# Performance work log

Measured on AMD Instinct MI355X. Metric: run time of the kernel, lower is better.

Reference implementation:

```python
import jax, jax.numpy as jnp
import numpy as np

N_NODES = 16384
N_EDGES = 65536
B = 256
L = 1000
BN_EPS = 1e-5


def _bn_last(h, g, b, m, v):
    # BatchNorm1d in eval mode over last (feature) axis
    return (h - m) / jnp.sqrt(v + BN_EPS) * g + b


def _bn_chan(h, g, b, m, v):
    # BatchNorm1d in eval mode over channel axis of [N, C, W]
    inv = g / jnp.sqrt(v + BN_EPS)
    return (h - m[None, :, None]) * inv[None, :, None] + b[None, :, None]


def _conv1d(x, W, b):
    # x: [N, C, W], W: [O, I, K], stride 1, VALID
    y = jax.lax.conv_general_dilated(x, W, (1,), 'VALID',
                                     dimension_numbers=('NCH', 'OIH', 'NCH'))
    return y + b[None, :, None]


def _forward(x, g1_W1, g1_b1, g1_W2, g1_b2, gW1, gb1, gW2, gb2,
             bn_gamma, bn_beta, bn_mean, bn_var, fcxd_W, fcxd_b, embed,
             c1_W, c1_b, c2_W, c2_b, c3_W, c3_b,
             cbn_gamma, cbn_beta, cbn_mean, cbn_var, fcxc_W, fcxc_b,
             bnfc_gamma, bnfc_beta, bnfc_mean, bnfc_var,
             fc1_W, fc1_b, fc2_W, fc2_b, out_W, out_b,
             edge_index, batch, target):
    src, dst = edge_index[0], edge_index[1]
    # GIN layer 1: out_i = MLP(x_i + sum_{j->i} x_j)  (eps = 0)
    agg = jax.ops.segment_sum(x[src], dst, num_segments=N_NODES)
    h = x + agg
    h = jnp.maximum(h @ g1_W1 + g1_b1, 0.0) @ g1_W2 + g1_b2
    h = _bn_last(jnp.maximum(h, 0.0), bn_gamma[0], bn_beta[0], bn_mean[0], bn_var[0])
    # GIN layers 2..5 (stacked params)
    for i in range(4):
        agg = jax.ops.segment_sum(h[src], dst, num_segments=N_NODES)
        t = h + agg
        t = jnp.maximum(t @ gW1[i] + gb1[i], 0.0) @ gW2[i] + gb2[i]
        h = _bn_last(jnp.maximum(t, 0.0), bn_gamma[i + 1], bn_beta[i + 1],
                     bn_mean[i + 1], bn_var[i + 1])
    # global_add_pool over graph ids
    pooled = jax.ops.segment_sum(h, batch, num_segments=B)          # [B, 32]
    xd = jnp.maximum(pooled @ fcxd_W + fcxd_b, 0.0)                 # [B, 128] (dropout: eval)
    # protein branch
    emb = embed[target]                                             # [B, L, 128]
    xd2 = jnp.broadcast_to(xd[:, None, :], (B, L, xd.shape[-1]))
    xc = jnp.concatenate([emb, xd2], axis=-1).transpose(0, 2, 1)    # [B, 256, L]
    conv_params = [(c1_W, c1_b), (c2_W, c2_b), (c3_W, c3_b)]
    for i in range(3):
        xc = _conv1d(xc, conv_params[i][0], conv_params[i][1])
        xc = jnp.maximum(_bn_chan(xc, cbn_gamma[i], cbn_beta[i],
                                  cbn_mean[i], cbn_var[i]), 0.0)
    xcm = jnp.max(xc, axis=-1)                                      # global max pool -> [B, 32]
    xcf = jnp.maximum(_bn_last(xcm @ fcxc_W + fcxc_b,
                               bnfc_gamma, bnfc_beta, bnfc_mean, bnfc_var), 0.0)
    z = jnp.concatenate([xd, xcf], axis=1)                          # [B, 256]
    z = jnp.maximum(z @ fc1_W + fc1_b, 0.0)
    z = jnp.maximum(z @ fc2_W + fc2_b, 0.0)
    return z @ out_W + out_b                                        # [B, 1]


def setup_inputs() -> dict:
    key = jax.random.key(0)
    ks = list(jax.random.split(key, 48))
    it = iter(range(48))
    f32 = jnp.float32

    def rn(sh, s=0.1):
        return jax.random.normal(ks[next(it)], sh, dtype=f32) * s

    def un(sh):
        return jax.random.uniform(ks[next(it)], sh, dtype=f32, minval=0.5, maxval=1.5)

    inp = {}
    inp['x'] = jax.random.normal(ks[next(it)], (N_NODES, 78), dtype=f32)
    inp['edge_index'] = jax.random.randint(ks[next(it)], (2, N_EDGES), 0, N_NODES, dtype=jnp.int32)
    inp['batch'] = jnp.sort(jax.random.randint(ks[next(it)], (N_NODES,), 0, B, dtype=jnp.int32))
    inp['target'] = jax.random.randint(ks[next(it)], (B, L), 0, 26, dtype=jnp.int32)
    inp['g1_W1'] = rn((78, 32)); inp['g1_b1'] = rn((32,))
    inp['g1_W2'] = rn((32, 32)); inp['g1_b2'] = rn((32,))
    inp['gW1'] = rn((4, 32, 32)); inp['gb1'] = rn((4, 32))
    inp['gW2'] = rn((4, 32, 32)); inp['gb2'] = rn((4, 32))
    inp['bn_gamma'] = un((5, 32)); inp['bn_beta'] = rn((5, 32))
    inp['bn_mean'] = rn((5, 32)); inp['bn_var'] = un((5, 32))
    inp['fcxd_W'] = rn((32, 128)); inp['fcxd_b'] = rn((128,))
    inp['embed'] = rn((26, 128), 1.0)
    inp['c1_W'] = rn((32, 256, 16)); inp['c1_b'] = rn((32,))
    inp['c2_W'] = rn((32, 32, 16)); inp['c2_b'] = rn((32,))
    inp['c3_W'] = rn((32, 32, 16)); inp['c3_b'] = rn((32,))
    inp['cbn_gamma'] = un((3, 32)); inp['cbn_beta'] = rn((3, 32))
    inp['cbn_mean'] = rn((3, 32)); inp['cbn_var'] = un((3, 32))
    inp['fcxc_W'] = rn((32, 128)); inp['fcxc_b'] = rn((128,))
    inp['bnfc_gamma'] = un((128,)); inp['bnfc_beta'] = rn((128,))
    inp['bnfc_mean'] = rn((128,)); inp['bnfc_var'] = un((128,))
    inp['fc1_W'] = rn((256, 1024)); inp['fc1_b'] = rn((1024,))
    inp['fc2_W'] = rn((1024, 256)); inp['fc2_b'] = rn((256,))
    inp['out_W'] = rn((256, 1)); inp['out_b'] = rn((1,))
    return inp


def reference(x, edge_index, batch, target, g1_W1, g1_b1, g1_W2, g1_b2,
              gW1, gb1, gW2, gb2, bn_gamma, bn_beta, bn_mean, bn_var,
              fcxd_W, fcxd_b, embed, c1_W, c1_b, c2_W, c2_b, c3_W, c3_b,
              cbn_gamma, cbn_beta, cbn_mean, cbn_var, fcxc_W, fcxc_b,
              bnfc_gamma, bnfc_beta, bnfc_mean, bnfc_var,
              fc1_W, fc1_b, fc2_W, fc2_b, out_W, out_b):
    return _forward(x, g1_W1, g1_b1, g1_W2, g1_b2, gW1, gb1, gW2, gb2,
                    bn_gamma, bn_beta, bn_mean, bn_var, fcxd_W, fcxd_b, embed,
                    c1_W, c1_b, c2_W, c2_b, c3_W, c3_b,
                    cbn_gamma, cbn_beta, cbn_mean, cbn_var, fcxc_W, fcxc_b,
                    bnfc_gamma, bnfc_beta, bnfc_mean, bnfc_var,
                    fc1_W, fc1_b, fc2_W, fc2_b, out_W, out_b,
                    edge_index, batch, target)
```

## Files before the change

kernel.cpp:

```cpp
#include <hip/hip_runtime.h>
#include <hip/hip_bf16.h>

typedef __hip_bfloat16 bf16;
__device__ __forceinline__ float b2f(bf16 v){ return __bfloat162float(v); }

typedef __attribute__((ext_vector_type(8))) short s8v;
typedef __attribute__((ext_vector_type(4))) float f4v;

#define N_NODES 16384
#define N_EDGES 65536
#define NB 256
#define LSEQ 1000
#define BN_EPS 1e-5f
#define W1O 985
#define W2O 970
#define W3O 955

__device__ int g_isf32;

__device__ __forceinline__ float LD(const void* p, int i, int f){
    return f ? ((const float*)p)[i] : b2f(((const bf16*)p)[i]);
}

__device__ __forceinline__ unsigned short f2b(float x){
    unsigned u = __float_as_uint(x);
    return (unsigned short)((u + 0x7FFFu + ((u >> 16) & 1u)) >> 16);
}
__device__ __forceinline__ float bb2f(unsigned short h){
    return __uint_as_float(((unsigned)h) << 16);
}

__global__ void k_dtype(const void* x){
    if (threadIdx.x != 0 || blockIdx.x != 0) return;
    const unsigned short* u = (const unsigned short*)x;
    int insane = 0;
    for (int i = 0; i < 512; i++){
        unsigned short h = u[i];
        int ex = (h >> 7) & 0xFF;
        if (!(h == 0 || (ex >= 96 && ex <= 142))) insane++;
    }
    g_isf32 = (insane > 50) ? 1 : 0;
}

__device__ float g_hA[N_NODES*32];
__device__ float g_hB[N_NODES*32];
__device__ float g_xd[NB*128];
__device__ float g_P[16*26*32];
__device__ float g_wsum[32*128];
__device__ float g_xdb[NB*32];
__device__ float g_xcm[NB*32];
__device__ __attribute__((aligned(16))) unsigned short g_wf[2][32768];
__device__ int g_deg[N_NODES];
__device__ int g_cur[N_NODES];
__device__ int g_rowptr[N_NODES + 1];
__device__ int g_csrc[N_EDGES];
__device__ int g_gstart[NB + 1];

__global__ void k_zero(){
    int i = blockIdx.x*256 + threadIdx.x;
    if (i < N_NODES) g_deg[i] = 0;
    else g_xcm[i - N_NODES] = 0.f;
}

__global__ void k_count(const int* __restrict__ ei){
    int e = blockIdx.x*256 + threadIdx.x;
    atomicAdd(&g_deg[ei[N_EDGES + e]], 1);
}
__global__ __launch_bounds__(1024) void k_scan(){
    __shared__ int part[1024];
    int t = threadIdx.x;
    int base = t*16;
    int s = 0;
    #pragma unroll
    for (int i = 0; i < 16; i++) s += g_deg[base + i];
    part[t] = s;
    __syncthreads();
    for (int off = 1; off < 1024; off <<= 1){
        int v = (t >= off) ? part[t - off] : 0;
        __syncthreads();
        part[t] += v;
        __syncthreads();
    }
    int run = (t == 0) ? 0 : part[t - 1];
    for (int i = 0; i < 16; i++){
        g_rowptr[base + i] = run;
        g_cur[base + i] = run;
        run += g_deg[base + i];
    }
    if (t == 1023) g_rowptr[N_NODES] = run;
}
__global__ void k_fill(const int* __restrict__ ei){
    int e = blockIdx.x*256 + threadIdx.x;
    int d = ei[N_EDGES + e];
    int slot = atomicAdd(&g_cur[d], 1);
    g_csrc[slot] = ei[e];
}
__global__ void k_ranges(const int* __restrict__ batch){
    int b = threadIdx.x;
    int lo = 0, hi = N_NODES;
    while (lo < hi){ int mid = (lo + hi) >> 1; if (batch[mid] < b) lo = mid + 1; else hi = mid; }
    g_gstart[b] = lo;
    if (b == 0) g_gstart[NB] = N_NODES;
}

__global__ void k_wpack(const void* w2, const void* w3){
    const int F = g_isf32;
    int idx = blockIdx.x*256 + threadIdx.x;
    int sel = idx >> 15;
    int r = idx & 32767;
    int j = r & 7;
    int lane = (r >> 3) & 63;
    int hl = (r >> 9) & 1;
    int ogrp = (r >> 10) & 1;
    int ktg = r >> 11;
    int c = (lane >> 4)*8 + j;
    int o = ogrp*16 + (lane & 15);
    const void* Wt = sel ? w3 : w2;
    float wv = LD(Wt, o*512 + c*16 + ktg, F);
    unsigned short h = f2b(wv);
    g_wf[sel][r] = hl ? f2b(wv - bb2f(h)) : h;
}


__global__ __launch_bounds__(256) void k_proj78(const void* x, const void* W1)
{
    const int F = g_isf32;
    __shared__ float sW1[78*32];
    __shared__ float sx[8][78];
    int tid = threadIdx.x;
    for (int i = tid; i < 78*32; i += 256) sW1[i] = LD(W1, i, F);
    int nodeBase = blockIdx.x * 8;
    for (int i = tid; i < 8*78; i += 256){
        int ln = i / 78, f = i - ln*78;
        sx[ln][f] = LD(x, (nodeBase + ln)*78 + f, F);
    }
    __syncthreads();
    int ln = tid >> 5, j = tid & 31;
    float a = 0.f;
    #pragma unroll 6
    for (int i = 0; i < 78; i++) a += sx[ln][i] * sW1[i*32 + j];
    g_hA[(nodeBase + ln)*32 + j] = a;
}

__device__ __forceinline__ float csr_gather(const float* hin, int n, int j){
    int rs = g_rowptr[n];
    int deg = g_rowptr[n + 1] - rs;
    float agg = 0.f;
    for (int base = 0; base < deg; base += 32){
        int cnt = deg - base; if (cnt > 32) cnt = 32;
        int myidx = (j < cnt) ? g_csrc[rs + base + j] : 0;
        for (int e = 0; e < cnt; e++){
            int src = __shfl(myidx, e, 32);
            agg += hin[src*32 + j];
        }
    }
    return agg;
}

__global__ __launch_bounds__(256) void k_gin1b(
    const void* b1, const void* W2, const void* b2,
    const void* bng, const void* bnb, const void* bnm, const void* bnv)
{
    const int F = g_isf32;
    __shared__ float sW2[32*32];
    __shared__ float sb1[32], sb2[32], sA[32], sB[32];
    __shared__ float st[8][32];
    int tid = threadIdx.x;
    for (int i = tid; i < 1024; i += 256) sW2[i] = LD(W2, i, F);
    if (tid < 32){
        sb1[tid] = LD(b1, tid, F); sb2[tid] = LD(b2, tid, F);
        float inv = LD(bng, tid, F) * rsqrtf(LD(bnv, tid, F) + BN_EPS);
        sA[tid] = inv;
        sB[tid] = LD(bnb, tid, F) - LD(bnm, tid, F) * inv;
    }
    __syncthreads();
    int ln = tid >> 5, j = tid & 31;
    int n = blockIdx.x*8 + ln;
    float agg = csr_gather(g_hA, n, j);
    st[ln][j] = fmaxf(g_hA[n*32 + j] + agg + sb1[j], 0.f);
    __syncthreads();
    float t2 = sb2[j];
    #pragma unroll
    for (int i = 0; i < 32; i++) t2 += st[ln][i] * sW2[i*32 + j];
    t2 = fmaxf(t2, 0.f);
    g_hB[n*32 + j] = t2 * sA[j] + sB[j];
}

__global__ __launch_bounds__(256) void k_gin32L(
    const void* W1, const void* b1, const void* W2, const void* b2,
    const void* bng, const void* bnb, const void* bnm, const void* bnv, int l)
{
    const int F = g_isf32;
    const float* hin = (l & 1) ? g_hA : g_hB;
    float* hout = (l & 1) ? g_hB : g_hA;
    const int oW = l*1024, ob = l*32, obn = (l+1)*32;
    __shared__ float sW1[32*32], sW2[32*32];
    __shared__ float sb1[32], sb2[32], sA[32], sB[32];
    __shared__ float sh[8][32], st[8][32];
    int tid = threadIdx.x;
    for (int i = tid; i < 1024; i += 256){ sW1[i] = LD(W1, oW + i, F); sW2[i] = LD(W2, oW + i, F); }
    if (tid < 32){
        sb1[tid] = LD(b1, ob + tid, F); sb2[tid] = LD(b2, ob + tid, F);
        float inv = LD(bng, obn + tid, F) * rsqrtf(LD(bnv, obn + tid, F) + BN_EPS);
        sA[tid] = inv;
        sB[tid] = LD(bnb, obn + tid, F) - LD(bnm, obn + tid, F) * inv;
    }
    int ln = tid >> 5, j = tid & 31;
    int n = blockIdx.x*8 + ln;
    float agg = csr_gather(hin, n, j);
    sh[ln][j] = hin[n*32 + j] + agg;
    __syncthreads();
    float t1 = sb1[j];
    #pragma unroll
    for (int i = 0; i < 32; i++) t1 += sh[ln][i] * sW1[i*32 + j];
    st[ln][j] = fmaxf(t1, 0.f);
    __syncthreads();
    float t2 = sb2[j];
    #pragma unroll
    for (int i = 0; i < 32; i++) t2 += st[ln][i] * sW2[i*32 + j];
    t2 = fmaxf(t2, 0.f);
    hout[n*32 + j] = t2 * sA[j] + sB[j];
}

__global__ __launch_bounds__(256) void k_poolxd(const void* W, const void* bias,
                                                const void* c1b){
    const int F = g_isf32;
    __shared__ float red[8][32];
    __shared__ float sxd[128];
    int b = blockIdx.x, tid = threadIdx.x;
    int j = tid & 31, sub = tid >> 5;
    int s = g_gstart[b], e = g_gstart[b + 1];
    float a = 0.f;
    for (int n = s + sub; n < e; n += 8) a += g_hB[n*32 + j];
    red[sub][j] = a;
    __syncthreads();
    if (sub == 0){
        red[0][j] = red[0][j] + red[1][j] + red[2][j] + red[3][j]
                  + red[4][j] + red[5][j] + red[6][j] + red[7][j];
    }
    __syncthreads();
    if (tid < 128){
        float acc = LD(bias, tid, F);
        #pragma unroll
        for (int i = 0; i < 32; i++) acc += red[0][i] * LD(W, i*128 + tid, F);
        float xdv = fmaxf(acc, 0.f);
        g_xd[b*128 + tid] = xdv;
        sxd[tid] = xdv;
    }
    __syncthreads();
    if (tid < 32){
        float a2 = LD(c1b, tid, F);
        for (int c = 0; c < 128; c++) a2 += sxd[c] * g_wsum[tid*128 + c];
        g_xdb[b*32 + tid] = a2;
    }
}


__global__ void k_Pw(const void* embed, const void* c1W){
    const int F = g_isf32;
    if (blockIdx.x < 52){
        int idx = blockIdx.x*256 + threadIdx.x;
        if (idx >= 16*26*32) return;
        int o = idx & 31;
        int t = (idx >> 5) % 26;
        int k = idx / (32*26);
        float a = 0.f;
        for (int c = 0; c < 128; c++)
            a += LD(embed, t*128 + c, F) * LD(c1W, o*4096 + c*16 + k, F);
        g_P[(k*26 + t)*32 + o] = a;
    } else {
        int idx = (blockIdx.x - 52)*256 + threadIdx.x;
        int o = idx >> 7, c = idx & 127;
        float a = 0.f;
        #pragma unroll
        for (int k = 0; k < 16; k++) a += LD(c1W, o*4096 + (128 + c)*16 + k, F);
        g_wsum[o*128 + c] = a;
    }
}


#define FT_W 128
#define C1R 160
#define C2R 144
#define CPAD 40
#define STGN 176

__global__ __launch_bounds__(512) void k_cfuse(
    const int* __restrict__ target,
    const void* g, const void* be, const void* m, const void* v,
    const void* c2b, const void* c3b)
{
    const int F = g_isf32;
    __shared__ int stg[STGN];
    __shared__ __attribute__((aligned(16))) unsigned short sC1h[C1R*CPAD];
    __shared__ __attribute__((aligned(16))) unsigned short sC1l[C1R*CPAD];
    __shared__ __attribute__((aligned(16))) unsigned short sC2h[C2R*CPAD];
    __shared__ __attribute__((aligned(16))) unsigned short sC2l[C2R*CPAD];
    __shared__ float sxb[32], sA1[32], sB1[32], sSc2[32], sOf2[32], sSc3[32], sOf3[32];
    int b = blockIdx.x >> 3;
    int tile = blockIdx.x & 7;
    int wbase = tile * FT_W;
    int tid = threadIdx.x;

    for (int i = tid; i < STGN; i += 512){
        int gi = wbase + i;
        stg[i] = (gi < LSEQ) ? target[b*LSEQ + gi] : 0;
    }
    if (tid < 32){
        sxb[tid] = g_xdb[b*32 + tid];
        float i1 = LD(g, tid, F) * rsqrtf(LD(v, tid, F) + BN_EPS);
        sA1[tid] = i1;
        sB1[tid] = LD(be, tid, F) - LD(m, tid, F) * i1;
        float i2 = LD(g, 32 + tid, F) * rsqrtf(LD(v, 32 + tid, F) + BN_EPS);
        sSc2[tid] = i2;
        sOf2[tid] = LD(be, 32 + tid, F) + (LD(c2b, tid, F) - LD(m, 32 + tid, F)) * i2;
        float i3 = LD(g, 64 + tid, F) * rsqrtf(LD(v, 64 + tid, F) + BN_EPS);
        sSc3[tid] = i3;
        sOf3[tid] = LD(be, 64 + tid, F) + (LD(c3b, tid, F) - LD(m, 64 + tid, F)) * i3;
    }
    __syncthreads();

    {
        int o = tid & 31, rsub = tid >> 5;
        for (int r = rsub; r < C1R; r += 16){
            float val = 0.f;
            if (wbase + r < W1O){
                float a = sxb[o];
                #pragma unroll
                for (int k = 0; k < 16; k++)
                    a += g_P[(k*26 + stg[r + k])*32 + o];
                val = fmaxf(a * sA1[o] + sB1[o], 0.f);
            }
            unsigned short h = f2b(val);
            sC1h[r*CPAD + o] = h;
            sC1l[r*CPAD + o] = f2b(val - bb2f(h));
        }
    }
    __syncthreads();

    int lane = tid & 63;
    int wv = tid >> 6;
    int ml = lane & 15, quad = lane >> 4;
    int ogrp = wv & 1;
    int part = wv >> 1;
    int oo = ogrp*16 + ml;

    {
        const s8v* wfb = (const s8v*)&g_wf[0][0] + ogrp*128 + lane;
        int nmt = (part == 0) ? 3 : 2;
        f4v acc[3];
        #pragma unroll
        for (int i = 0; i < 3; i++) acc[i] = (f4v){0.f,0.f,0.f,0.f};
        s8v nbh = wfb[0], nbl = wfb[64];
        for (int ktg = 0; ktg < 16; ktg++){
            s8v bh = nbh, bl = nbl;
            if (ktg < 15){ nbh = wfb[(ktg+1)*256]; nbl = wfb[(ktg+1)*256 + 64]; }
            #pragma unroll
            for (int i = 0; i < 3; i++){
                if (i < nmt){
                    int row = (part + 4*i)*16 + ml + ktg;
                    int aidx = row*CPAD + quad*8;
                    s8v ah = *(const s8v*)&sC1h[aidx];
                    s8v al = *(const s8v*)&sC1l[aidx];
                    acc[i] = __builtin_amdgcn_mfma_f32_16x16x32_bf16(ah, bh, acc[i], 0, 0, 0);
                    acc[i] = __builtin_amdgcn_mfma_f32_16x16x32_bf16(ah, bl, acc[i], 0, 0, 0);
                    acc[i] = __builtin_amdgcn_mfma_f32_16x16x32_bf16(al, bh, acc[i], 0, 0, 0);
                }
            }
        }
        float sc = sSc2[oo], of = sOf2[oo];
        #pragma unroll
        for (int i = 0; i < 3; i++){
            if (i < nmt){
                int mt = part + 4*i;
                f4v a = acc[i];
                float ys[4] = {a.x, a.y, a.z, a.w};
                #pragma unroll
                for (int rr = 0; rr < 4; rr++){
                    int row = mt*16 + quad*4 + rr;
                    float y = fmaxf(ys[rr]*sc + of, 0.f);
                    unsigned short h = f2b(y);
                    sC2h[row*CPAD + oo] = h;
                    sC2l[row*CPAD + oo] = f2b(y - bb2f(h));
                }
            }
        }
    }
    __syncthreads();

    {
        const s8v* wfb = (const s8v*)&g_wf[1][0] + ogrp*128 + lane;
        f4v acc[2];
        #pragma unroll
        for (int i = 0; i < 2; i++) acc[i] = (f4v){0.f,0.f,0.f,0.f};
        s8v nbh = wfb[0], nbl = wfb[64];
        for (int ktg = 0; ktg < 16; ktg++){
            s8v bh = nbh, bl = nbl;
            if (ktg < 15){ nbh = wfb[(ktg+1)*256]; nbl = wfb[(ktg+1)*256 + 64]; }
            #pragma unroll
            for (int i = 0; i < 2; i++){
                int row = (part + 4*i)*16 + ml + ktg;
                int aidx = row*CPAD + quad*8;
                s8v ah = *(const s8v*)&sC2h[aidx];
                s8v al = *(const s8v*)&sC2l[aidx];
                acc[i] = __builtin_amdgcn_mfma_f32_16x16x32_bf16(ah, bh, acc[i], 0, 0, 0);
                acc[i] = __builtin_amdgcn_mfma_f32_16x16x32_bf16(ah, bl, acc[i], 0, 0, 0);
                acc[i] = __builtin_amdgcn_mfma_f32_16x16x32_bf16(al, bh, acc[i], 0, 0, 0);
            }
        }
        float sc = sSc3[oo], of = sOf3[oo];
        #pragma unroll
        for (int i = 0; i < 2; i++){
            int mt = part + 4*i;
            int w0 = wbase + mt*16 + quad*4;
            f4v a = acc[i];
            float y0 = fmaxf(a.x*sc + of, 0.f);
            float y1 = fmaxf(a.y*sc + of, 0.f);
            float y2 = fmaxf(a.z*sc + of, 0.f);
            float y3 = fmaxf(a.w*sc + of, 0.f);
            if (w0 < W3O){
                float mx = y0;
                if (w0+1 < W3O) mx = fmaxf(mx, y1);
                if (w0+2 < W3O) mx = fmaxf(mx, y2);
                if (w0+3 < W3O) mx = fmaxf(mx, y3);
                atomicMax((int*)&g_xcm[b*32 + oo], __float_as_int(mx));
            }
        }
    }
}


__global__ __launch_bounds__(1024) void k_tail(
    const void* fcxcW, const void* fcxcb,
    const void* bg, const void* bb, const void* bm, const void* bv,
    const void* fc1W, const void* fc1b,
    const void* fc2W, const void* fc2b,
    const void* outW, const void* outb, void* out)
{
    const int F = g_isf32;
    __shared__ float sz[256];
    __shared__ float z1s[1024];
    __shared__ float sp[4][256];
    int b = blockIdx.x, t = threadIdx.x;
    if (t < 128) sz[t] = g_xd[b*128 + t];
    else if (t < 256){
        int j = t - 128;
        float a = LD(fcxcb, j, F);
        #pragma unroll
        for (int i = 0; i < 32; i++) a += g_xcm[b*32 + i] * LD(fcxcW, i*128 + j, F);
        float inv = LD(bg, j, F) * rsqrtf(LD(bv, j, F) + BN_EPS);
        a = (a - LD(bm, j, F)) * inv + LD(bb, j, F);
        sz[t] = fmaxf(a, 0.f);
    }
    __syncthreads();
    float a = LD(fc1b, t, F);
    for (int i = 0; i < 256; i++) a += sz[i] * LD(fc1W, i*1024 + t, F);
    z1s[t] = fmaxf(a, 0.f);
    __syncthreads();
    int j = t & 255, kq = t >> 8;
    float a2 = 0.f;
    #pragma unroll 8
    for (int i = 0; i < 256; i++)
        a2 += z1s[kq*256 + i] * LD(fc2W, (kq*256 + i)*256 + j, F);
    sp[kq][j] = a2;
    __syncthreads();
    if (t < 256){
        float z2 = fmaxf(sp[0][t] + sp[1][t] + sp[2][t] + sp[3][t] + LD(fc2b, t, F), 0.f);
        sp[0][t] = z2 * LD(outW, t, F);
    }
    __syncthreads();
    for (int s = 128; s > 0; s >>= 1){
        if (t < s) sp[0][t] += sp[0][t + s];
        __syncthreads();
    }
    if (t == 0){
        float r = sp[0][0] + LD(outb, 0, F);
        if (F) ((float*)out)[b] = r;
        else   ((bf16*)out)[b] = __float2bfloat16(r);
    }
}


extern "C" void kernel_launch(void* const* d_in, const int* in_sizes, int n_in,
                              void* d_out, int out_size, void* d_ws, size_t ws_size,
                              hipStream_t stream)
{
    (void)in_sizes; (void)n_in; (void)out_size; (void)d_ws; (void)ws_size;
    const void* x      = d_in[0];
    const int*  ei     = (const int*)d_in[1];
    const int*  batch  = (const int*)d_in[2];
    const int*  target = (const int*)d_in[3];
    const void* g1W1 = d_in[4];  const void* g1b1 = d_in[5];
    const void* g1W2 = d_in[6];  const void* g1b2 = d_in[7];
    const void* gW1  = d_in[8];  const void* gb1  = d_in[9];
    const void* gW2  = d_in[10]; const void* gb2  = d_in[11];
    const void* bng  = d_in[12]; const void* bnb  = d_in[13];
    const void* bnm  = d_in[14]; const void* bnv  = d_in[15];
    const void* fcxdW = d_in[16]; const void* fcxdb = d_in[17];
    const void* embed = d_in[18];
    const void* c1W = d_in[19]; const void* c1b = d_in[20];
    const void* c2W = d_in[21]; const void* c2b = d_in[22];
    const void* c3W = d_in[23]; const void* c3b = d_in[24];
    const void* cbng = d_in[25]; const void* cbnb = d_in[26];
    const void* cbnm = d_in[27]; const void* cbnv = d_in[28];
    const void* fcxcW = d_in[29]; const void* fcxcb = d_in[30];
    const void* bnfcg = d_in[31]; const void* bnfcb = d_in[32];
    const void* bnfcm = d_in[33]; const void* bnfcv = d_in[34];
    const void* fc1W = d_in[35]; const void* fc1b = d_in[36];
    const void* fc2W = d_in[37]; const void* fc2b = d_in[38];
    const void* outW = d_in[39]; const void* outb = d_in[40];

    k_dtype<<<1, 64, 0, stream>>>(x);
    k_wpack<<<256, 256, 0, stream>>>(c2W, c3W);
    k_Pw<<<68, 256, 0, stream>>>(embed, c1W);

    k_zero<<<(N_NODES + NB*32)/256, 256, 0, stream>>>();
    k_count<<<N_EDGES/256, 256, 0, stream>>>(ei);
    k_scan<<<1, 1024, 0, stream>>>();
    k_fill<<<N_EDGES/256, 256, 0, stream>>>(ei);
    k_ranges<<<1, 256, 0, stream>>>(batch);

    k_proj78<<<N_NODES/8, 256, 0, stream>>>(x, g1W1);
    k_gin1b<<<N_NODES/8, 256, 0, stream>>>(g1b1, g1W2, g1b2, bng, bnb, bnm, bnv);
    for (int l = 0; l < 4; l++){
        k_gin32L<<<N_NODES/8, 256, 0, stream>>>(gW1, gb1, gW2, gb2,
                                                bng, bnb, bnm, bnv, l);
    }
    k_poolxd<<<NB, 256, 0, stream>>>(fcxdW, fcxdb, c1b);
    k_cfuse<<<NB*8, 512, 0, stream>>>(target, cbng, cbnb, cbnm, cbnv, c2b, c3b);
    k_tail<<<NB, 1024, 0, stream>>>(fcxcW, fcxcb, bnfcg, bnfcb, bnfcm, bnfcv,
                                    fc1W, fc1b, fc2W, fc2b, outW, outb, d_out);
}
```

Measured before the change: 431.5 us.

## Merge preprocessing and GIN layers into one cooperative persistent kernel

Result: slower. 796.7 us (+84.7%).

```diff
diff --git a/kernel.cpp b/kernel.cpp
--- a/kernel.cpp
+++ b/kernel.cpp
@@ -1,5 +1,8 @@
 #include <hip/hip_runtime.h>
 #include <hip/hip_bf16.h>
+#include <hip/hip_cooperative_groups.h>
+
+namespace cg = cooperative_groups;
 
 typedef __hip_bfloat16 bf16;
 __device__ __forceinline__ float b2f(bf16 v){ return __bfloat162float(v); }
@@ -275,6 +278,250 @@
         #pragma unroll
         for (int k = 0; k < 16; k++) a += LD(c1W, o*4096 + (128 + c)*16 + k, F);
         g_wsum[o*128 + c] = a;
+    }
+}
+
+
+struct CoopArgs {
+    const void* x; const int* ei; const int* batch;
+    const void* g1W1; const void* g1b1; const void* g1W2; const void* g1b2;
+    const void* gW1;  const void* gb1;  const void* gW2;  const void* gb2;
+    const void* bng;  const void* bnb;  const void* bnm;  const void* bnv;
+    const void* fcxdW; const void* fcxdb;
+    const void* embed; const void* c1W; const void* c1b;
+    const void* c2W;   const void* c3W;
+};
+
+__global__ __launch_bounds__(256) void k_coop(CoopArgs a)
+{
+    cg::grid_group grid = cg::this_grid();
+
+    union SMem {
+        struct { float W1[78*32]; float x[16][78]; } p0;
+        struct { float W1[1024]; float W2[1024];
+                 float b1[32], b2[32], A[32], B[32];
+                 float h[8][32]; float t[8][32]; } gin;
+        struct { int part[256]; } scan;
+        struct { float red[8][32]; float xd[128]; } pool;
+    };
+    __shared__ __attribute__((aligned(16))) SMem sm;
+    __shared__ int s_cnt;
+
+    const int tid = threadIdx.x;
+    const int bid = blockIdx.x;
+    const int nblk = gridDim.x;
+    const int ln = tid >> 5, j = tid & 31;
+
+    if (tid == 0) s_cnt = 0;
+    __syncthreads();
+    {
+        const unsigned short* u = (const unsigned short*)a.x;
+        int bad = 0;
+        for (int i = tid; i < 512; i += 256){
+            unsigned short h = u[i];
+            int ex = (h >> 7) & 0xFF;
+            if (!(h == 0 || (ex >= 96 && ex <= 142))) bad++;
+        }
+        if (bad) atomicAdd(&s_cnt, bad);
+    }
+    __syncthreads();
+    const int F = (s_cnt > 50) ? 1 : 0;
+    if (bid == 0 && tid == 0) g_isf32 = F;
+
+    {
+        int vb = (bid + 512) % nblk;
+        for (int i = vb*256 + tid; i < N_NODES + NB*32; i += nblk*256){
+            if (i < N_NODES) g_deg[i] = 0; else g_xcm[i - N_NODES] = 0.f;
+        }
+    }
+    {
+        for (int idx = bid*256 + tid; idx < 65536; idx += nblk*256){
+            int sel = idx >> 15;
+            int r = idx & 32767;
+            int jj = r & 7;
+            int lane = (r >> 3) & 63;
+            int hl = (r >> 9) & 1;
+            int ogrp = (r >> 10) & 1;
+            int ktg = r >> 11;
+            int c = (lane >> 4)*8 + jj;
+            int o = ogrp*16 + (lane & 15);
+            const void* Wt = sel ? a.c3W : a.c2W;
+            float wv = LD(Wt, o*512 + c*16 + ktg, F);
+            unsigned short h = f2b(wv);
+            g_wf[sel][r] = hl ? f2b(wv - bb2f(h)) : h;
+        }
+    }
+    {
+        int vb = (bid + 256) % nblk;
+        for (int idx = vb*256 + tid; idx < 16*26*32; idx += nblk*256){
+            int k = idx & 15, o = (idx >> 4) & 31, t = idx >> 9;
+            float acc = 0.f;
+            for (int c = 0; c < 128; c++)
+                acc += LD(a.embed, t*128 + c, F) * LD(a.c1W, o*4096 + c*16 + k, F);
+            g_P[(k*26 + t)*32 + o] = acc;
+        }
+    }
+    {
+        int vb = (bid + 320) % nblk;
+        for (int idx = vb*256 + tid; idx < 4096; idx += nblk*256){
+            int o = idx >> 7, c = idx & 127;
+            float acc = 0.f;
+            #pragma unroll
+            for (int k = 0; k < 16; k++) acc += LD(a.c1W, o*4096 + (128 + c)*16 + k, F);
+            g_wsum[o*128 + c] = acc;
+        }
+    }
+    {
+        int vb = (bid + 400) % nblk;
+        for (int b = vb*256 + tid; b < NB; b += nblk*256){
+            int lo = 0, hi = N_NODES;
+            while (lo < hi){ int mid = (lo + hi) >> 1; if (a.batch[mid] < b) lo = mid + 1; else hi = mid; }
+            g_gstart[b] = lo;
+            if (b == 0) g_gstart[NB] = N_NODES;
+        }
+    }
+    for (int i = tid; i < 78*32; i += 256) sm.p0.W1[i] = LD(a.g1W1, i, F);
+    for (int grp = bid; grp < N_NODES/16; grp += nblk){
+        __syncthreads();
+        int nodeBase = grp*16;
+        for (int i = tid; i < 16*78; i += 256){
+            int l2 = i/78, f = i - l2*78;
+            sm.p0.x[l2][f] = LD(a.x, (nodeBase + l2)*78 + f, F);
+        }
+        __syncthreads();
+        #pragma unroll
+        for (int half = 0; half < 2; half++){
+            int lnn = half*8 + ln;
+            float acc = 0.f;
+            #pragma unroll 6
+            for (int i = 0; i < 78; i++) acc += sm.p0.x[lnn][i] * sm.p0.W1[i*32 + j];
+            g_hA[(nodeBase + lnn)*32 + j] = acc;
+        }
+    }
+    grid.sync();
+
+    for (int e = bid*256 + tid; e < N_EDGES; e += nblk*256)
+        atomicAdd(&g_deg[a.ei[N_EDGES + e]], 1);
+    grid.sync();
+
+    if (bid == 0){
+        int base = tid*64, s = 0;
+        for (int i = 0; i < 64; i++) s += g_deg[base + i];
+        sm.scan.part[tid] = s;
+        __syncthreads();
+        for (int off = 1; off < 256; off <<= 1){
+            int v = (tid >= off) ? sm.scan.part[tid - off] : 0;
+            __syncthreads();
+            sm.scan.part[tid] += v;
+            __syncthreads();
+        }
+        int run = (tid == 0) ? 0 : sm.scan.part[tid - 1];
+        for (int i = 0; i < 64; i++){
+            g_rowptr[base + i] = run;
+            g_cur[base + i] = run;
+            run += g_deg[base + i];
+        }
+        if (tid == 255) g_rowptr[N_NODES] = run;
+    }
+    grid.sync();
+
+    for (int e = bid*256 + tid; e < N_EDGES; e += nblk*256){
+        int d = a.ei[N_EDGES + e];
+        int slot = atomicAdd(&g_cur[d], 1);
+        g_csrc[slot] = a.ei[e];
+    }
+    grid.sync();
+
+    for (int i = tid; i < 1024; i += 256) sm.gin.W2[i] = LD(a.g1W2, i, F);
+    if (tid < 32){
+        sm.gin.b1[tid] = LD(a.g1b1, tid, F);
+        sm.gin.b2[tid] = LD(a.g1b2, tid, F);
+        float inv = LD(a.bng, tid, F) * rsqrtf(LD(a.bnv, tid, F) + BN_EPS);
+        sm.gin.A[tid] = inv;
+        sm.gin.B[tid] = LD(a.bnb, tid, F) - LD(a.bnm, tid, F) * inv;
+    }
+    for (int grp = bid; grp < N_NODES/16; grp += nblk){
+        #pragma unroll
+        for (int half = 0; half < 2; half++){
+            __syncthreads();
+            int n = grp*16 + half*8 + ln;
+            float agg = csr_gather(g_hA, n, j);
+            sm.gin.t[ln][j] = fmaxf(g_hA[n*32 + j] + agg + sm.gin.b1[j], 0.f);
+            __syncthreads();
+            float t2 = sm.gin.b2[j];
+            #pragma unroll
+            for (int i = 0; i < 32; i++) t2 += sm.gin.t[ln][i] * sm.gin.W2[i*32 + j];
+            t2 = fmaxf(t2, 0.f);
+            g_hB[n*32 + j] = t2 * sm.gin.A[j] + sm.gin.B[j];
+        }
+    }
+    grid.sync();
+
+    for (int l = 0; l < 4; l++){
+        const float* hin = (l & 1) ? g_hA : g_hB;
+        float* hout = (l & 1) ? g_hB : g_hA;
+        const int oW = l*1024, ob = l*32, obn = (l+1)*32;
+        for (int i = tid; i < 1024; i += 256){
+            sm.gin.W1[i] = LD(a.gW1, oW + i, F);
+            sm.gin.W2[i] = LD(a.gW2, oW + i, F);
+        }
+        if (tid < 32){
+            sm.gin.b1[tid] = LD(a.gb1, ob + tid, F);
+            sm.gin.b2[tid] = LD(a.gb2, ob + tid, F);
+            float inv = LD(a.bng, obn + tid, F) * rsqrtf(LD(a.bnv, obn + tid, F) + BN_EPS);
+            sm.gin.A[tid] = inv;
+            sm.gin.B[tid] = LD(a.bnb, obn + tid, F) - LD(a.bnm, obn + tid, F) * inv;
+        }
+        for (int grp = bid; grp < N_NODES/16; grp += nblk){
+            #pragma unroll
+            for (int half = 0; half < 2; half++){
+                __syncthreads();
+                int n = grp*16 + half*8 + ln;
+                float agg = csr_gather(hin, n, j);
+                sm.gin.h[ln][j] = hin[n*32 + j] + agg;
+                __syncthreads();
+                float t1 = sm.gin.b1[j];
+                #pragma unroll
+                for (int i = 0; i < 32; i++) t1 += sm.gin.h[ln][i] * sm.gin.W1[i*32 + j];
+                sm.gin.t[ln][j] = fmaxf(t1, 0.f);
+                __syncthreads();
+                float t2 = sm.gin.b2[j];
+                #pragma unroll
+                for (int i = 0; i < 32; i++) t2 += sm.gin.t[ln][i] * sm.gin.W2[i*32 + j];
+                t2 = fmaxf(t2, 0.f);
+                hout[n*32 + j] = t2 * sm.gin.A[j] + sm.gin.B[j];
+            }
+        }
+        grid.sync();
+    }
+
+    for (int b = bid; b < NB; b += nblk){
+        __syncthreads();
+        int s = g_gstart[b], e = g_gstart[b + 1];
+        float acc = 0.f;
+        for (int n = s + ln; n < e; n += 8) acc += g_hB[n*32 + j];
+        sm.pool.red[ln][j] = acc;
+        __syncthreads();
+        if (ln == 0){
+            sm.pool.red[0][j] = sm.pool.red[0][j] + sm.pool.red[1][j] + sm.pool.red[2][j]
+                              + sm.pool.red[3][j] + sm.pool.red[4][j] + sm.pool.red[5][j]
+                              + sm.pool.red[6][j] + sm.pool.red[7][j];
+        }
+        __syncthreads();
+        if (tid < 128){
+            float acc2 = LD(a.fcxdb, tid, F);
+            #pragma unroll
+            for (int i = 0; i < 32; i++) acc2 += sm.pool.red[0][i] * LD(a.fcxdW, i*128 + tid, F);
+            float xdv = fmaxf(acc2, 0.f);
+            g_xd[b*128 + tid] = xdv;
+            sm.pool.xd[tid] = xdv;
+        }
+        __syncthreads();
+        if (tid < 32){
+            float a2 = LD(a.c1b, tid, F);
+            for (int c = 0; c < 128; c++) a2 += sm.pool.xd[c] * g_wsum[tid*128 + c];
+            g_xdb[b*32 + tid] = a2;
+        }
     }
 }
 
@@ -510,23 +757,54 @@
     const void* fc2W = d_in[37]; const void* fc2b = d_in[38];
     const void* outW = d_in[39]; const void* outb = d_in[40];
 
-    k_dtype<<<1, 64, 0, stream>>>(x);
-    k_wpack<<<256, 256, 0, stream>>>(c2W, c3W);
-    k_Pw<<<68, 256, 0, stream>>>(embed, c1W);
-
-    k_zero<<<(N_NODES + NB*32)/256, 256, 0, stream>>>();
-    k_count<<<N_EDGES/256, 256, 0, stream>>>(ei);
-    k_scan<<<1, 1024, 0, stream>>>();
-    k_fill<<<N_EDGES/256, 256, 0, stream>>>(ei);
-    k_ranges<<<1, 256, 0, stream>>>(batch);
-
-    k_proj78<<<N_NODES/8, 256, 0, stream>>>(x, g1W1);
-    k_gin1b<<<N_NODES/8, 256, 0, stream>>>(g1b1, g1W2, g1b2, bng, bnb, bnm, bnv);
-    for (int l = 0; l < 4; l++){
-        k_gin32L<<<N_NODES/8, 256, 0, stream>>>(gW1, gb1, gW2, gb2,
-                                                bng, bnb, bnm, bnv, l);
-    }
-    k_poolxd<<<NB, 256, 0, stream>>>(fcxdW, fcxdb, c1b);
+    static int s_coopGrid = -2;
+    if (s_coopGrid == -2){
+        hipDeviceProp_t prop{};
+        int dev = 0;
+        if (hipGetDevice(&dev) == hipSuccess &&
+            hipGetDeviceProperties(&prop, dev) == hipSuccess &&
+            prop.cooperativeLaunch){
+            int nb = 0;
+            hipError_t e2 = hipOccupancyMaxActiveBlocksPerMultiprocessor(
+                                &nb, reinterpret_cast<const void*>(&k_coop), 256, 0);
+            if (e2 == hipSuccess && nb >= 1){
+                long cap = (long)nb * (long)prop.multiProcessorCount;
+                s_coopGrid = (int)(cap < 1024 ? cap : 1024);
+            } else s_coopGrid = -1;
+        } else s_coopGrid = -1;
+    }
+
+    bool coop_ok = false;
+    if (s_coopGrid > 0){
+        CoopArgs ca = { x, ei, batch, g1W1, g1b1, g1W2, g1b2,
+                        gW1, gb1, gW2, gb2, bng, bnb, bnm, bnv,
+                        fcxdW, fcxdb, embed, c1W, c1b, c2W, c3W };
+        void* kargs[] = { (void*)&ca };
+        hipError_t le = hipLaunchCooperativeKernel(
+            reinterpret_cast<const void*>(&k_coop),
+            dim3(s_coopGrid), dim3(256), kargs, 0, stream);
+        if (le == hipSuccess) coop_ok = true;
+        else s_coopGrid = -1;
+    }
+
+    if (!coop_ok){
+        k_dtype<<<1, 64, 0, stream>>>(x);
+        k_wpack<<<256, 256, 0, stream>>>(c2W, c3W);
+        k_Pw<<<68, 256, 0, stream>>>(embed, c1W);
+        k_zero<<<(N_NODES + NB*32)/256, 256, 0, stream>>>();
+        k_count<<<N_EDGES/256, 256, 0, stream>>>(ei);
+        k_scan<<<1, 1024, 0, stream>>>();
+        k_fill<<<N_EDGES/256, 256, 0, stream>>>(ei);
+        k_ranges<<<1, 256, 0, stream>>>(batch);
+        k_proj78<<<N_NODES/8, 256, 0, stream>>>(x, g1W1);
+        k_gin1b<<<N_NODES/8, 256, 0, stream>>>(g1b1, g1W2, g1b2, bng, bnb, bnm, bnv);
+        for (int l = 0; l < 4; l++){
+            k_gin32L<<<N_NODES/8, 256, 0, stream>>>(gW1, gb1, gW2, gb2,
+                                                    bng, bnb, bnm, bnv, l);
+        }
+        k_poolxd<<<NB, 256, 0, stream>>>(fcxdW, fcxdb, c1b);
+    }
+
     k_cfuse<<<NB*8, 512, 0, stream>>>(target, cbng, cbnb, cbnm, cbnv, c2b, c3b);
     k_tail<<<NB, 1024, 0, stream>>>(fcxcW, fcxcb, bnfcg, bnfcb, bnfcm, bnfcv,
                                     fc1W, fc1b, fc2W, fc2b, outW, outb, d_out);
```
